# Kernel tuning notes

Hardware: AMD Instinct MI355X
Metric: run time of the kernel (lower is better)

Reference implementation:

```python
import jax, jax.numpy as jnp
import numpy as np

D_MODEL = 1024
NUM_HEADS = 16
DEPTH = D_MODEL // NUM_HEADS
B, S = 4, 1024


def setup_inputs() -> dict:
    key = jax.random.key(0)
    ks = jax.random.split(key, 12)
    sc = 1.0 / np.sqrt(D_MODEL)
    return {
        "v": jax.random.normal(ks[0], (B, S, D_MODEL), jnp.float32),
        "k": jax.random.normal(ks[1], (B, S, D_MODEL), jnp.float32),
        "q": jax.random.normal(ks[2], (B, S, D_MODEL), jnp.float32),
        "mask": jnp.zeros((B, 1, 1, S), jnp.float32),
        "adjoin_matrix": jax.random.normal(ks[3], (B, 1, S, S), jnp.float32),
        "wq_w": jax.random.normal(ks[4], (D_MODEL, D_MODEL), jnp.float32) * sc,
        "wq_b": jnp.zeros((D_MODEL,), jnp.float32),
        "wk_w": jax.random.normal(ks[5], (D_MODEL, D_MODEL), jnp.float32) * sc,
        "wk_b": jnp.zeros((D_MODEL,), jnp.float32),
        "wv_w": jax.random.normal(ks[6], (D_MODEL, D_MODEL), jnp.float32) * sc,
        "wv_b": jnp.zeros((D_MODEL,), jnp.float32),
        "dense_w": jax.random.normal(ks[7], (D_MODEL, D_MODEL), jnp.float32) * sc,
        "dense_b": jnp.zeros((D_MODEL,), jnp.float32),
    }


def _split_heads(x, batch):
    # [B, S, D] -> [B, H, S, depth]
    return x.reshape(batch, -1, NUM_HEADS, DEPTH).transpose(0, 2, 1, 3)


def reference(v, k, q, mask, adjoin_matrix,
              wq_w, wq_b, wk_w, wk_b, wv_w, wv_b, dense_w, dense_b):
    batch = q.shape[0]
    # torch nn.Linear: y = x @ W^T + b
    qh = _split_heads(q @ wq_w.T + wq_b, batch)
    kh = _split_heads(k @ wk_w.T + wk_b, batch)
    vh = _split_heads(v @ wv_w.T + wv_b, batch)

    logits = jnp.einsum('bhqd,bhkd->bhqk', qh, kh) / jnp.sqrt(
        jnp.asarray(DEPTH, qh.dtype))
    logits = logits + mask * (-1e9) + adjoin_matrix
    attn = jax.nn.softmax(logits, axis=-1).astype(qh.dtype)
    # dropout p=0 -> identity at inference
    ctx = jnp.einsum('bhqk,bhkd->bhqd', attn, vh)  # [B,H,S,depth]
    concat = ctx.transpose(0, 2, 1, 3).reshape(batch, -1, D_MODEL)
    out = concat @ dense_w.T + dense_b
    return out, attn
```

## Files before the change

### kernel.cpp

```cpp
#include <hip/hip_runtime.h>
#include <hip/hip_bf16.h>
#include <cstdint>
#include <cstddef>

#define B_ 4
#define S_ 1024
#define D_ 1024
#define H_ 16
#define DEPTH_ 64
#define M_ (B_*S_)

typedef __attribute__((ext_vector_type(4))) float f32x4;
typedef __attribute__((ext_vector_type(8))) __bf16 bf16x8;
typedef __attribute__((ext_vector_type(8))) unsigned short u16x8;
typedef __attribute__((ext_vector_type(4))) unsigned short u16x4;

typedef const __attribute__((address_space(1))) unsigned int GU32;
typedef __attribute__((address_space(3))) unsigned int LU32;

__device__ __forceinline__ unsigned short f2bf(float f) {
  unsigned int u = __builtin_bit_cast(unsigned int, f);
  u += 0x7FFFu + ((u >> 16) & 1u);
  return (unsigned short)(u >> 16);
}

__device__ __forceinline__ float bf2f(unsigned short v) {
  unsigned int u = (unsigned int)v << 16;
  return __builtin_bit_cast(float, u);
}

struct CvtAll { const float* s[7]; unsigned short* d[7]; };

__device__ __forceinline__ void cvt_body(const float* __restrict__ s,
                                         unsigned short* __restrict__ d, int i) {
  const f32x4* sp = (const f32x4*)s + (size_t)i * 2;
  f32x4 a = sp[0], b = sp[1];
  u16x8 o;
  o[0]=f2bf(a[0]); o[1]=f2bf(a[1]); o[2]=f2bf(a[2]); o[3]=f2bf(a[3]);
  o[4]=f2bf(b[0]); o[5]=f2bf(b[1]); o[6]=f2bf(b[2]); o[7]=f2bf(b[3]);
  *((u16x8*)d + i) = o;
}

__global__ void cvt_all_kernel(CvtAll a) {
  int bi = blockIdx.x, seg, i;
  if (bi < 6144) { seg = bi >> 11;              i = ((bi & 2047) << 8) + threadIdx.x; }
  else           { int t = bi - 6144; seg = 3 + (t >> 9); i = ((t & 511) << 8) + threadIdx.x; }
  cvt_body(a.s[seg], a.d[seg], i);
}

__device__ __forceinline__ void gemm_body(
    const unsigned short* __restrict__ A,
    const unsigned short* __restrict__ Bm,
    unsigned short* __restrict__ Obf,
    float* __restrict__ Of32,
    const float* __restrict__ bias,
    int N, int K, float scale, int biasRow, int m0, int n0)
{
  __shared__ unsigned short As[128*32];
  __shared__ unsigned short Bs[128*32];
  const int tid  = threadIdx.x;
  const int lane = tid & 63;
  const int w    = tid >> 6;
  const int wm   = w >> 1, wn = w & 1;
  const int fr   = lane & 15, kg = lane >> 4;

  f32x4 acc[4][4];
  #pragma unroll
  for (int i = 0; i < 4; ++i)
    #pragma unroll
    for (int j = 0; j < 4; ++j)
      acc[i][j] = (f32x4)0.0f;

  const int o0 = tid * 16,        o1 = (256 + tid) * 16;
  const int r0 = o0 >> 6,         c0 = (o0 & 63) >> 1;
  const int r1 = o1 >> 6,         c1 = (o1 & 63) >> 1;
  const int lds0 = (w * 64) * 16;
  const int lds1 = (256 + w * 64) * 16;

  const int nkt = K >> 5;
  for (int kt = 0; kt < nkt; ++kt) {
    const int kk = kt * 32;
    __builtin_amdgcn_global_load_lds((GU32*)(A  + (size_t)(m0 + r0) * K + kk + c0),
                                     (LU32*)((char*)As + lds0), 16, 0, 0);
    __builtin_amdgcn_global_load_lds((GU32*)(A  + (size_t)(m0 + r1) * K + kk + c1),
                                     (LU32*)((char*)As + lds1), 16, 0, 0);
    __builtin_amdgcn_global_load_lds((GU32*)(Bm + (size_t)(n0 + r0) * K + kk + c0),
                                     (LU32*)((char*)Bs + lds0), 16, 0, 0);
    __builtin_amdgcn_global_load_lds((GU32*)(Bm + (size_t)(n0 + r1) * K + kk + c1),
                                     (LU32*)((char*)Bs + lds1), 16, 0, 0);
    __syncthreads();

    bf16x8 af[4], bf[4];
    #pragma unroll
    for (int i = 0; i < 4; ++i)
      af[i] = *(const bf16x8*)&As[(wm * 64 + i * 16 + fr) * 32 + kg * 8];
    #pragma unroll
    for (int j = 0; j < 4; ++j)
      bf[j] = *(const bf16x8*)&Bs[(wn * 64 + j * 16 + fr) * 32 + kg * 8];
    #pragma unroll
    for (int i = 0; i < 4; ++i)
      #pragma unroll
      for (int j = 0; j < 4; ++j)
        acc[i][j] = __builtin_amdgcn_mfma_f32_16x16x32_bf16(af[i], bf[j], acc[i][j], 0, 0, 0);
    __syncthreads();
  }

  #pragma unroll
  for (int i = 0; i < 4; ++i) {
    const int rowb = m0 + wm * 64 + i * 16 + kg * 4;
    #pragma unroll
    for (int j = 0; j < 4; ++j) {
      const int col = n0 + wn * 64 + j * 16 + fr;
      const float bcol = biasRow ? 0.0f : bias[col];
      #pragma unroll
      for (int r = 0; r < 4; ++r) {
        const int row = rowb + r;
        const float bv = biasRow ? bias[row] : bcol;
        const float val = (acc[i][j][r] + bv) * scale;
        if (Obf) Obf[(size_t)row * N + col] = f2bf(val);
        else     Of32[(size_t)row * N + col] = val;
      }
    }
  }
}

struct GemmSet { const unsigned short* A; const unsigned short* Bm;
                 unsigned short* O; const float* bias; };

__launch_bounds__(256)
__global__ void qkv_gemm(GemmSet s0, GemmSet s1, GemmSet s2) {
  const int z = blockIdx.y;
  GemmSet s = (z == 0) ? s0 : (z == 1) ? s1 : s2;
  int m0, n0, N; float scale; int biasRow;
  if (z < 2) { m0 = (blockIdx.x & 31) * 128; n0 = (blockIdx.x >> 5) * 128;
               N = D_; scale = (z == 0) ? 0.125f : 1.0f; biasRow = 0; }
  else       { m0 = (blockIdx.x & 7) * 128;  n0 = (blockIdx.x >> 3) * 128;
               N = M_; scale = 1.0f; biasRow = 1; }
  gemm_body(s.A, s.Bm, s.O, nullptr, s.bias, N, D_, scale, biasRow, m0, n0);
}

__launch_bounds__(256)
__global__ void dense_gemm(const unsigned short* __restrict__ A,
                           const unsigned short* __restrict__ Bm,
                           float* __restrict__ O, const float* __restrict__ bias) {
  gemm_body(A, Bm, nullptr, O, bias, D_, D_, 1.0f, 0,
            blockIdx.x * 128, blockIdx.y * 128);
}

__launch_bounds__(512, 4)
__global__ void attn_kernel(const unsigned short* __restrict__ qp,
                            const unsigned short* __restrict__ kp,
                            const unsigned short* __restrict__ vt,
                            const float* __restrict__ mask,
                            const float* __restrict__ adjoin,
                            float* __restrict__ attn_out,
                            unsigned short* __restrict__ ctx)
{
  __shared__ __align__(16) char L[81920];
  char* const Pb = L;
  char* const Rg = L + 32768;

  const int tid = threadIdx.x, lane = tid & 63, w = tid >> 6;
  const int fr = lane & 15, kg = lane >> 4;
  const int fd = w & 3, kh = w >> 2;
  const int frsw = (fr & 7) << 4;
  const int r8 = lane >> 3;
  const int c7p = (((lane & 7) ^ r8) << 4);

  char* const Wb  = Rg + w * 6144;
  char* const Ks0 = Wb,        * const Ks1 = Wb + 2048;
  char* const Ab0 = Wb + 4096, * const Ab1 = Wb + 5120;

  const int i_ = blockIdx.x;
  const int bh = (i_ & 7) * 8 + ((i_ >> 3) & 7);
  const int qt = i_ >> 6;
  const int b = bh >> 4, h = bh & 15;
  const int q0 = qt * 16;
  const int kw = w * 128;

  const char* kG = (const char*)(kp + (size_t)b * S_ * D_ + h * DEPTH_);
  const char* aG = (const char*)(adjoin + (size_t)b * S_ * S_ + (size_t)q0 * S_);
  const char* vG = (const char*)(vt + (size_t)h * DEPTH_ * M_ + (size_t)b * S_);
  const char* mG = (const char*)(mask + (size_t)b * S_);

  auto stageK = [&](int t, char* dst) {
    #pragma unroll
    for (int j = 0; j < 2; ++j)
      __builtin_amdgcn_global_load_lds(
          (GU32*)(kG + (size_t)(kw + t * 16 + j * 8 + r8) * 2048 + c7p),
          (LU32*)(dst + j * 1024 + lane * 16), 16, 0, 0);
  };
  auto stageA = [&](int t, char* dst) {
    __builtin_amdgcn_global_load_lds(
        (GU32*)(aG + (size_t)(lane >> 2) * 4096 + kw * 4 + t * 64 + (lane & 3) * 16),
        (LU32*)(dst + lane * 16), 16, 0, 0);
  };
  auto stageV = [&](int t, char* dst) {
    #pragma unroll
    for (int j = 0; j < 2; ++j)
      __builtin_amdgcn_global_load_lds(
          (GU32*)(vG + (size_t)(fd * 16 + j * 8 + r8) * 8192 + kh * 1024 + t * 128 + c7p),
          (LU32*)(dst + j * 1024 + lane * 16), 16, 0, 0);
  };

  const unsigned short* qrow = qp + ((size_t)b * S_ + q0 + fr) * D_ + h * DEPTH_;
  bf16x8 qf0 = *(const bf16x8*)&qrow[kg * 8];
  bf16x8 qf1 = *(const bf16x8*)&qrow[32 + kg * 8];
  f32x4 mreg[8];
  #pragma unroll
  for (int t = 0; t < 8; ++t)
    mreg[t] = *(const f32x4*)(mG + kw * 4 + t * 64 + kg * 16);
  asm volatile("" ::: "memory");

  stageK(0, Ks0); stageA(0, Ab0);
  stageK(1, Ks1); stageA(1, Ab1);
  asm volatile("s_waitcnt vmcnt(3)" ::: "memory");
  __builtin_amdgcn_sched_barrier(0);

  float ls = 0.0f;

  #pragma unroll
  for (int t = 0; t < 8; ++t) {
    if (t == 7)     asm volatile("s_waitcnt vmcnt(2)" ::: "memory");
    else if (t > 0) asm volatile("s_waitcnt vmcnt(3)" ::: "memory");
    __builtin_amdgcn_sched_barrier(0);

    const char* kb = (t & 1) ? Ks1 : Ks0;
    const char* ab = (t & 1) ? Ab1 : Ab0;
    bf16x8 kf0 = *(const bf16x8*)(kb + fr * 128 + ((kg * 16) ^ frsw));
    bf16x8 kf1 = *(const bf16x8*)(kb + fr * 128 + ((64 + kg * 16) ^ frsw));
    f32x4 a4  = *(const f32x4*)(ab + fr * 64 + kg * 16);

    asm volatile("s_waitcnt lgkmcnt(0)" ::: "memory");
    __builtin_amdgcn_sched_barrier(0);

    if (t < 6)      { stageK(t + 2, (t & 1) ? Ks1 : Ks0);
                      stageA(t + 2, (t & 1) ? Ab1 : Ab0); }
    else if (t == 6)  stageV(0, Ks0);
    else              stageV(1, Ks1);

    f32x4 s = (f32x4)0.0f;
    s = __builtin_amdgcn_mfma_f32_16x16x32_bf16(kf0, qf0, s, 0, 0, 0);
    s = __builtin_amdgcn_mfma_f32_16x16x32_bf16(kf1, qf1, s, 0, 0, 0);

    f32x4 p;
    #pragma unroll
    for (int r = 0; r < 4; ++r)
      p[r] = __expf(s[r] + a4[r] + mreg[t][r] * (-1e9f));
    ls += (p[0] + p[1]) + (p[2] + p[3]);
    u16x4 pk;
    #pragma unroll
    for (int r = 0; r < 4; ++r) pk[r] = f2bf(p[r]);
    *(u16x4*)(Pb + fr * 2048 + ((kw * 2 + t * 32 + kg * 8) ^ frsw)) = pk;
  }

  ls += __shfl_xor(ls, 16);
  ls += __shfl_xor(ls, 32);
  if (lane < 16) *(float*)(Ab0 + lane * 4) = ls;

  asm volatile("s_waitcnt lgkmcnt(0)" ::: "memory");
  __builtin_amdgcn_s_barrier();
  __builtin_amdgcn_sched_barrier(0);

  f32x4 cacc = (f32x4)0.0f;
  #pragma unroll
  for (int t = 0; t < 8; ++t) {
    if (t == 7) asm volatile("s_waitcnt vmcnt(0)" ::: "memory");
    else        asm volatile("s_waitcnt vmcnt(2)" ::: "memory");
    __builtin_amdgcn_sched_barrier(0);

    const char* vb = (t & 1) ? Ks1 : Ks0;
    bf16x8 vf0 = *(const bf16x8*)(vb + fr * 128 + ((kg * 16) ^ frsw));
    bf16x8 vf1 = *(const bf16x8*)(vb + fr * 128 + ((64 + kg * 16) ^ frsw));
    bf16x8 pf0 = *(const bf16x8*)(Pb + fr * 2048 + ((kh * 1024 + t * 128 + kg * 16) ^ frsw));
    bf16x8 pf1 = *(const bf16x8*)(Pb + fr * 2048 + ((kh * 1024 + t * 128 + 64 + kg * 16) ^ frsw));

    asm volatile("s_waitcnt lgkmcnt(0)" ::: "memory");
    __builtin_amdgcn_sched_barrier(0);

    if (t < 6) stageV(t + 2, (t & 1) ? Ks1 : Ks0);

    cacc = __builtin_amdgcn_mfma_f32_16x16x32_bf16(vf0, pf0, cacc, 0, 0, 0);
    cacc = __builtin_amdgcn_mfma_f32_16x16x32_bf16(vf1, pf1, cacc, 0, 0, 0);
  }

  if (w >= 4) *(f32x4*)(Ab1 + lane * 16) = cacc;
  asm volatile("s_waitcnt lgkmcnt(0)" ::: "memory");
  __builtin_amdgcn_s_barrier();
  __builtin_amdgcn_sched_barrier(0);

  if (w < 4) {
    f32x4 red = *(const f32x4*)(Rg + (w + 4) * 6144 + 5120 + lane * 16);
    #pragma unroll
    for (int r = 0; r < 4; ++r) cacc[r] += red[r];
    float gs = 0.0f;
    #pragma unroll
    for (int w2 = 0; w2 < 8; ++w2)
      gs += *(const float*)(Rg + w2 * 6144 + 4096 + fr * 4);
    const float giC = 1.0f / gs;
    u16x4 cv;
    #pragma unroll
    for (int r = 0; r < 4; ++r) cv[r] = f2bf(cacc[r] * giC);
    *(u16x4*)&ctx[((size_t)b * S_ + q0 + fr) * D_ + h * DEPTH_ + fd * 16 + kg * 4] = cv;
  }

  #pragma unroll
  for (int j = 0; j < 2; ++j) {
    const int row = w * 2 + j;
    float gs = 0.0f;
    #pragma unroll
    for (int w2 = 0; w2 < 8; ++w2)
      gs += *(const float*)(Rg + w2 * 6144 + 4096 + row * 4);
    const float g = 1.0f / gs;
    const char* pr = Pb + row * 2048;
    const int rs = (row & 7) << 4;
    float* ao = attn_out + ((size_t)bh * S_ + q0 + row) * S_;
    #pragma unroll
    for (int half = 0; half < 2; ++half) {
      u16x8 pv = *(const u16x8*)(pr + ((half * 1024 + lane * 16) ^ rs));
      f32x4 o0, o1;
      #pragma unroll
      for (int e = 0; e < 4; ++e) { o0[e] = bf2f(pv[e]) * g; o1[e] = bf2f(pv[4 + e]) * g; }
      __builtin_nontemporal_store(o0, (f32x4*)(ao + half * 512 + lane * 8));
      __builtin_nontemporal_store(o1, (f32x4*)(ao + half * 512 + lane * 8 + 4));
    }
  }
}

extern "C" void kernel_launch(void* const* d_in, const int* in_sizes, int n_in,
                              void* d_out, int out_size, void* d_ws, size_t ws_size,
                              hipStream_t stream)
{
  const float* v_in   = (const float*)d_in[0];
  const float* k_in   = (const float*)d_in[1];
  const float* q_in   = (const float*)d_in[2];
  const float* mask   = (const float*)d_in[3];
  const float* adjoin = (const float*)d_in[4];
  const float* wq_w   = (const float*)d_in[5];
  const float* wq_b   = (const float*)d_in[6];
  const float* wk_w   = (const float*)d_in[7];
  const float* wk_b   = (const float*)d_in[8];
  const float* wv_w   = (const float*)d_in[9];
  const float* wv_b   = (const float*)d_in[10];
  const float* wd_w   = (const float*)d_in[11];
  const float* wd_b   = (const float*)d_in[12];

  unsigned short* xq  = (unsigned short*)d_ws;
  unsigned short* xk  = xq  + (size_t)M_ * D_;
  unsigned short* xv  = xk  + (size_t)M_ * D_;
  unsigned short* wqb = xv  + (size_t)M_ * D_;
  unsigned short* wkb = wqb + (size_t)D_ * D_;
  unsigned short* wvb = wkb + (size_t)D_ * D_;
  unsigned short* wdb = wvb + (size_t)D_ * D_;
  unsigned short* qp  = wdb + (size_t)D_ * D_;
  unsigned short* kp  = qp  + (size_t)M_ * D_;
  unsigned short* vt  = kp  + (size_t)M_ * D_;
  unsigned short* ctx = vt  + (size_t)M_ * D_;

  float* out  = (float*)d_out;
  float* attn = out + (size_t)B_ * S_ * D_;

  CvtAll ca;
  ca.s[0] = q_in; ca.s[1] = k_in; ca.s[2] = v_in;
  ca.s[3] = wq_w; ca.s[4] = wk_w; ca.s[5] = wv_w; ca.s[6] = wd_w;
  ca.d[0] = xq;   ca.d[1] = xk;   ca.d[2] = xv;
  ca.d[3] = wqb;  ca.d[4] = wkb;  ca.d[5] = wvb;  ca.d[6] = wdb;
  cvt_all_kernel<<<8192, 256, 0, stream>>>(ca);

  GemmSet sq{xq,  wqb, qp, wq_b};
  GemmSet sk{xk,  wkb, kp, wk_b};
  GemmSet sv{wvb, xv,  vt, wv_b};
  qkv_gemm<<<dim3(256, 3), 256, 0, stream>>>(sq, sk, sv);

  attn_kernel<<<B_ * H_ * (S_ / 16), 512, 0, stream>>>(qp, kp, vt, mask, adjoin, attn, ctx);

  dense_gemm<<<dim3(32, 8), 256, 0, stream>>>(ctx, wdb, out, wd_b);
}
```

Measured before the change: 186.8 us.

## Load K, adjoin, mask and V straight into registers instead of LDS staging

```diff
diff --git a/kernel.cpp b/kernel.cpp
--- a/kernel.cpp
+++ b/kernel.cpp
@@ -156,20 +156,15 @@
                             float* __restrict__ attn_out,
                             unsigned short* __restrict__ ctx)
 {
-  __shared__ __align__(16) char L[81920];
+  __shared__ __align__(16) char L[37376];
   char* const Pb = L;
-  char* const Rg = L + 32768;
+  float* const ssum = (float*)(L + 32768);
+  char* const Red = L + 33280;
 
   const int tid = threadIdx.x, lane = tid & 63, w = tid >> 6;
   const int fr = lane & 15, kg = lane >> 4;
   const int fd = w & 3, kh = w >> 2;
   const int frsw = (fr & 7) << 4;
-  const int r8 = lane >> 3;
-  const int c7p = (((lane & 7) ^ r8) << 4);
-
-  char* const Wb  = Rg + w * 6144;
-  char* const Ks0 = Wb,        * const Ks1 = Wb + 2048;
-  char* const Ab0 = Wb + 4096, * const Ab1 = Wb + 5120;
 
   const int i_ = blockIdx.x;
   const int bh = (i_ & 7) * 8 + ((i_ >> 3) & 7);
@@ -183,121 +178,77 @@
   const char* vG = (const char*)(vt + (size_t)h * DEPTH_ * M_ + (size_t)b * S_);
   const char* mG = (const char*)(mask + (size_t)b * S_);
 
-  auto stageK = [&](int t, char* dst) {
-    #pragma unroll
-    for (int j = 0; j < 2; ++j)
-      __builtin_amdgcn_global_load_lds(
-          (GU32*)(kG + (size_t)(kw + t * 16 + j * 8 + r8) * 2048 + c7p),
-          (LU32*)(dst + j * 1024 + lane * 16), 16, 0, 0);
-  };
-  auto stageA = [&](int t, char* dst) {
-    __builtin_amdgcn_global_load_lds(
-        (GU32*)(aG + (size_t)(lane >> 2) * 4096 + kw * 4 + t * 64 + (lane & 3) * 16),
-        (LU32*)(dst + lane * 16), 16, 0, 0);
-  };
-  auto stageV = [&](int t, char* dst) {
-    #pragma unroll
-    for (int j = 0; j < 2; ++j)
-      __builtin_amdgcn_global_load_lds(
-          (GU32*)(vG + (size_t)(fd * 16 + j * 8 + r8) * 8192 + kh * 1024 + t * 128 + c7p),
-          (LU32*)(dst + j * 1024 + lane * 16), 16, 0, 0);
-  };
+  const char* kA = kG + (size_t)(kw + fr) * 2048 + kg * 16;
+  const char* aA = aG + (size_t)fr * 4096 + kw * 4 + kg * 16;
+  const char* mA = mG + kw * 4 + kg * 16;
+  const char* vA = vG + (size_t)(fd * 16 + fr) * 8192 + kh * 1024 + kg * 16;
 
   const unsigned short* qrow = qp + ((size_t)b * S_ + q0 + fr) * D_ + h * DEPTH_;
   bf16x8 qf0 = *(const bf16x8*)&qrow[kg * 8];
   bf16x8 qf1 = *(const bf16x8*)&qrow[32 + kg * 8];
-  f32x4 mreg[8];
-  #pragma unroll
-  for (int t = 0; t < 8; ++t)
-    mreg[t] = *(const f32x4*)(mG + kw * 4 + t * 64 + kg * 16);
-  asm volatile("" ::: "memory");
-
-  stageK(0, Ks0); stageA(0, Ab0);
-  stageK(1, Ks1); stageA(1, Ab1);
-  asm volatile("s_waitcnt vmcnt(3)" ::: "memory");
-  __builtin_amdgcn_sched_barrier(0);
-
+
+  bf16x8 kf0c = *(const bf16x8*)(kA);
+  bf16x8 kf1c = *(const bf16x8*)(kA + 64);
+  f32x4  a4c  = *(const f32x4*)(aA);
+  f32x4  m4c  = *(const f32x4*)(mA);
   float ls = 0.0f;
-
   #pragma unroll
   for (int t = 0; t < 8; ++t) {
-    if (t == 7)     asm volatile("s_waitcnt vmcnt(2)" ::: "memory");
-    else if (t > 0) asm volatile("s_waitcnt vmcnt(3)" ::: "memory");
-    __builtin_amdgcn_sched_barrier(0);
-
-    const char* kb = (t & 1) ? Ks1 : Ks0;
-    const char* ab = (t & 1) ? Ab1 : Ab0;
-    bf16x8 kf0 = *(const bf16x8*)(kb + fr * 128 + ((kg * 16) ^ frsw));
-    bf16x8 kf1 = *(const bf16x8*)(kb + fr * 128 + ((64 + kg * 16) ^ frsw));
-    f32x4 a4  = *(const f32x4*)(ab + fr * 64 + kg * 16);
-
-    asm volatile("s_waitcnt lgkmcnt(0)" ::: "memory");
-    __builtin_amdgcn_sched_barrier(0);
-
-    if (t < 6)      { stageK(t + 2, (t & 1) ? Ks1 : Ks0);
-                      stageA(t + 2, (t & 1) ? Ab1 : Ab0); }
-    else if (t == 6)  stageV(0, Ks0);
-    else              stageV(1, Ks1);
+    const int tn = (t < 7) ? t + 1 : 7;
+    bf16x8 kf0n = *(const bf16x8*)(kA + (size_t)tn * 32768);
+    bf16x8 kf1n = *(const bf16x8*)(kA + (size_t)tn * 32768 + 64);
+    f32x4  a4n  = *(const f32x4*)(aA + tn * 64);
+    f32x4  m4n  = *(const f32x4*)(mA + tn * 64);
 
     f32x4 s = (f32x4)0.0f;
-    s = __builtin_amdgcn_mfma_f32_16x16x32_bf16(kf0, qf0, s, 0, 0, 0);
-    s = __builtin_amdgcn_mfma_f32_16x16x32_bf16(kf1, qf1, s, 0, 0, 0);
+    s = __builtin_amdgcn_mfma_f32_16x16x32_bf16(kf0c, qf0, s, 0, 0, 0);
+    s = __builtin_amdgcn_mfma_f32_16x16x32_bf16(kf1c, qf1, s, 0, 0, 0);
 
     f32x4 p;
     #pragma unroll
     for (int r = 0; r < 4; ++r)
-      p[r] = __expf(s[r] + a4[r] + mreg[t][r] * (-1e9f));
+      p[r] = __expf(s[r] + a4c[r] + m4c[r] * (-1e9f));
     ls += (p[0] + p[1]) + (p[2] + p[3]);
     u16x4 pk;
     #pragma unroll
     for (int r = 0; r < 4; ++r) pk[r] = f2bf(p[r]);
     *(u16x4*)(Pb + fr * 2048 + ((kw * 2 + t * 32 + kg * 8) ^ frsw)) = pk;
+
+    kf0c = kf0n; kf1c = kf1n; a4c = a4n; m4c = m4n;
   }
 
   ls += __shfl_xor(ls, 16);
   ls += __shfl_xor(ls, 32);
-  if (lane < 16) *(float*)(Ab0 + lane * 4) = ls;
-
-  asm volatile("s_waitcnt lgkmcnt(0)" ::: "memory");
-  __builtin_amdgcn_s_barrier();
-  __builtin_amdgcn_sched_barrier(0);
+  if (lane < 16) ssum[lane * 8 + w] = ls;
+
+  __syncthreads();
 
   f32x4 cacc = (f32x4)0.0f;
+  bf16x8 vf0c = *(const bf16x8*)(vA);
+  bf16x8 vf1c = *(const bf16x8*)(vA + 64);
   #pragma unroll
   for (int t = 0; t < 8; ++t) {
-    if (t == 7) asm volatile("s_waitcnt vmcnt(0)" ::: "memory");
-    else        asm volatile("s_waitcnt vmcnt(2)" ::: "memory");
-    __builtin_amdgcn_sched_barrier(0);
-
-    const char* vb = (t & 1) ? Ks1 : Ks0;
-    bf16x8 vf0 = *(const bf16x8*)(vb + fr * 128 + ((kg * 16) ^ frsw));
-    bf16x8 vf1 = *(const bf16x8*)(vb + fr * 128 + ((64 + kg * 16) ^ frsw));
+    const int tn = (t < 7) ? t + 1 : 7;
+    bf16x8 vf0n = *(const bf16x8*)(vA + tn * 128);
+    bf16x8 vf1n = *(const bf16x8*)(vA + tn * 128 + 64);
     bf16x8 pf0 = *(const bf16x8*)(Pb + fr * 2048 + ((kh * 1024 + t * 128 + kg * 16) ^ frsw));
     bf16x8 pf1 = *(const bf16x8*)(Pb + fr * 2048 + ((kh * 1024 + t * 128 + 64 + kg * 16) ^ frsw));
-
-    asm volatile("s_waitcnt lgkmcnt(0)" ::: "memory");
-    __builtin_amdgcn_sched_barrier(0);
-
-    if (t < 6) stageV(t + 2, (t & 1) ? Ks1 : Ks0);
-
-    cacc = __builtin_amdgcn_mfma_f32_16x16x32_bf16(vf0, pf0, cacc, 0, 0, 0);
-    cacc = __builtin_amdgcn_mfma_f32_16x16x32_bf16(vf1, pf1, cacc, 0, 0, 0);
-  }
-
-  if (w >= 4) *(f32x4*)(Ab1 + lane * 16) = cacc;
-  asm volatile("s_waitcnt lgkmcnt(0)" ::: "memory");
-  __builtin_amdgcn_s_barrier();
-  __builtin_amdgcn_sched_barrier(0);
+    cacc = __builtin_amdgcn_mfma_f32_16x16x32_bf16(vf0c, pf0, cacc, 0, 0, 0);
+    cacc = __builtin_amdgcn_mfma_f32_16x16x32_bf16(vf1c, pf1, cacc, 0, 0, 0);
+    vf0c = vf0n; vf1c = vf1n;
+  }
+
+  if (w >= 4) *(f32x4*)(Red + fd * 1024 + lane * 16) = cacc;
+  __syncthreads();
 
   if (w < 4) {
-    f32x4 red = *(const f32x4*)(Rg + (w + 4) * 6144 + 5120 + lane * 16);
+    f32x4 red = *(const f32x4*)(Red + fd * 1024 + lane * 16);
     #pragma unroll
     for (int r = 0; r < 4; ++r) cacc[r] += red[r];
-    float gs = 0.0f;
-    #pragma unroll
-    for (int w2 = 0; w2 < 8; ++w2)
-      gs += *(const float*)(Rg + w2 * 6144 + 4096 + fr * 4);
-    const float giC = 1.0f / gs;
+    f32x4 sa = *(const f32x4*)&ssum[fr * 8];
+    f32x4 sb = *(const f32x4*)&ssum[fr * 8 + 4];
+    const float giC = 1.0f / ((sa[0] + sa[1]) + (sa[2] + sa[3]) +
+                              ((sb[0] + sb[1]) + (sb[2] + sb[3])));
     u16x4 cv;
     #pragma unroll
     for (int r = 0; r < 4; ++r) cv[r] = f2bf(cacc[r] * giC);
@@ -307,11 +258,10 @@
   #pragma unroll
   for (int j = 0; j < 2; ++j) {
     const int row = w * 2 + j;
-    float gs = 0.0f;
-    #pragma unroll
-    for (int w2 = 0; w2 < 8; ++w2)
-      gs += *(const float*)(Rg + w2 * 6144 + 4096 + row * 4);
-    const float g = 1.0f / gs;
+    f32x4 ta = *(const f32x4*)&ssum[row * 8];
+    f32x4 tb = *(const f32x4*)&ssum[row * 8 + 4];
+    const float g = 1.0f / ((ta[0] + ta[1]) + (ta[2] + ta[3]) +
+                            ((tb[0] + tb[1]) + (tb[2] + tb[3])));
     const char* pr = Pb + row * 2048;
     const int rs = (row & 7) << 4;
     float* ao = attn_out + ((size_t)bh * S_ + q0 + row) * S_;
```

After: 269.2 us. 44.1% more time.

## Deepen attention K/adjoin/V staging to four buffers with register prefetch

Applied to the files above, without the earlier changes.

```diff
diff --git a/kernel.cpp b/kernel.cpp
--- a/kernel.cpp
+++ b/kernel.cpp
@@ -147,7 +147,7 @@
             blockIdx.x * 128, blockIdx.y * 128);
 }
 
-__launch_bounds__(512, 4)
+__launch_bounds__(512, 2)
 __global__ void attn_kernel(const unsigned short* __restrict__ qp,
                             const unsigned short* __restrict__ kp,
                             const unsigned short* __restrict__ vt,
@@ -156,9 +156,11 @@
                             float* __restrict__ attn_out,
                             unsigned short* __restrict__ ctx)
 {
-  __shared__ __align__(16) char L[81920];
+  __shared__ __align__(16) char L[135680];
   char* const Pb = L;
   char* const Rg = L + 32768;
+  float* const Ssum = (float*)(L + 131072);
+  char* const Red = L + 131584;
 
   const int tid = threadIdx.x, lane = tid & 63, w = tid >> 6;
   const int fr = lane & 15, kg = lane >> 4;
@@ -167,9 +169,13 @@
   const int r8 = lane >> 3;
   const int c7p = (((lane & 7) ^ r8) << 4);
 
-  char* const Wb  = Rg + w * 6144;
-  char* const Ks0 = Wb,        * const Ks1 = Wb + 2048;
-  char* const Ab0 = Wb + 4096, * const Ab1 = Wb + 5120;
+  char* const Wb = Rg + w * 12288;
+  char* const Kb0 = Wb,         * const Kb1 = Wb + 2048;
+  char* const Kb2 = Wb + 4096,  * const Kb3 = Wb + 6144;
+  char* const Ab0 = Wb + 8192,  * const Ab1 = Wb + 9216;
+  char* const Ab2 = Wb + 10240, * const Ab3 = Wb + 11264;
+  char* const KB[4] = {Kb0, Kb1, Kb2, Kb3};
+  char* const AB[4] = {Ab0, Ab1, Ab2, Ab3};
 
   const int i_ = blockIdx.x;
   const int bh = (i_ & 7) * 8 + ((i_ >> 3) & 7);
@@ -212,92 +218,116 @@
     mreg[t] = *(const f32x4*)(mG + kw * 4 + t * 64 + kg * 16);
   asm volatile("" ::: "memory");
 
-  stageK(0, Ks0); stageA(0, Ab0);
-  stageK(1, Ks1); stageA(1, Ab1);
-  asm volatile("s_waitcnt vmcnt(3)" ::: "memory");
+  stageK(0, Kb0); stageA(0, Ab0);
+  stageK(1, Kb1); stageA(1, Ab1);
+  stageK(2, Kb2); stageA(2, Ab2);
+  stageK(3, Kb3); stageA(3, Ab3);
+  asm volatile("s_waitcnt vmcnt(9)" ::: "memory");
   __builtin_amdgcn_sched_barrier(0);
 
+  bf16x8 kf0c = *(const bf16x8*)(Kb0 + fr * 128 + ((kg * 16) ^ frsw));
+  bf16x8 kf1c = *(const bf16x8*)(Kb0 + fr * 128 + ((64 + kg * 16) ^ frsw));
+  f32x4  a4c  = *(const f32x4*)(Ab0 + fr * 64 + kg * 16);
+
   float ls = 0.0f;
 
   #pragma unroll
   for (int t = 0; t < 8; ++t) {
-    if (t == 7)     asm volatile("s_waitcnt vmcnt(2)" ::: "memory");
-    else if (t > 0) asm volatile("s_waitcnt vmcnt(3)" ::: "memory");
-    __builtin_amdgcn_sched_barrier(0);
-
-    const char* kb = (t & 1) ? Ks1 : Ks0;
-    const char* ab = (t & 1) ? Ab1 : Ab0;
-    bf16x8 kf0 = *(const bf16x8*)(kb + fr * 128 + ((kg * 16) ^ frsw));
-    bf16x8 kf1 = *(const bf16x8*)(kb + fr * 128 + ((64 + kg * 16) ^ frsw));
-    f32x4 a4  = *(const f32x4*)(ab + fr * 64 + kg * 16);
-
     asm volatile("s_waitcnt lgkmcnt(0)" ::: "memory");
     __builtin_amdgcn_sched_barrier(0);
 
-    if (t < 6)      { stageK(t + 2, (t & 1) ? Ks1 : Ks0);
-                      stageA(t + 2, (t & 1) ? Ab1 : Ab0); }
-    else if (t == 6)  stageV(0, Ks0);
-    else              stageV(1, Ks1);
+    if (t + 4 <= 7) { stageK(t + 4, KB[t & 3]); stageA(t + 4, AB[t & 3]); }
+
+    bf16x8 kf0n, kf1n; f32x4 a4n;
+    if (t < 7) {
+      if (t <= 3)      asm volatile("s_waitcnt vmcnt(9)" ::: "memory");
+      else if (t == 4) asm volatile("s_waitcnt vmcnt(6)" ::: "memory");
+      else if (t == 5) asm volatile("s_waitcnt vmcnt(3)" ::: "memory");
+      else             asm volatile("s_waitcnt vmcnt(0)" ::: "memory");
+      __builtin_amdgcn_sched_barrier(0);
+      const char* kb = KB[(t + 1) & 3];
+      const char* ab = AB[(t + 1) & 3];
+      kf0n = *(const bf16x8*)(kb + fr * 128 + ((kg * 16) ^ frsw));
+      kf1n = *(const bf16x8*)(kb + fr * 128 + ((64 + kg * 16) ^ frsw));
+      a4n  = *(const f32x4*)(ab + fr * 64 + kg * 16);
+    }
 
     f32x4 s = (f32x4)0.0f;
-    s = __builtin_amdgcn_mfma_f32_16x16x32_bf16(kf0, qf0, s, 0, 0, 0);
-    s = __builtin_amdgcn_mfma_f32_16x16x32_bf16(kf1, qf1, s, 0, 0, 0);
-
+    s = __builtin_amdgcn_mfma_f32_16x16x32_bf16(kf0c, qf0, s, 0, 0, 0);
+    s = __builtin_amdgcn_mfma_f32_16x16x32_bf16(kf1c, qf1, s, 0, 0, 0);
     f32x4 p;
     #pragma unroll
     for (int r = 0; r < 4; ++r)
-      p[r] = __expf(s[r] + a4[r] + mreg[t][r] * (-1e9f));
+      p[r] = __expf(s[r] + a4c[r] + mreg[t][r] * (-1e9f));
     ls += (p[0] + p[1]) + (p[2] + p[3]);
     u16x4 pk;
     #pragma unroll
     for (int r = 0; r < 4; ++r) pk[r] = f2bf(p[r]);
     *(u16x4*)(Pb + fr * 2048 + ((kw * 2 + t * 32 + kg * 8) ^ frsw)) = pk;
-  }
+
+    if (t < 7) { kf0c = kf0n; kf1c = kf1n; a4c = a4n; }
+  }
+
+  asm volatile("s_waitcnt lgkmcnt(0)" ::: "memory");
+  __builtin_amdgcn_sched_barrier(0);
+  stageV(0, Kb0); stageV(1, Kb1); stageV(2, Kb2); stageV(3, Kb3);
 
   ls += __shfl_xor(ls, 16);
   ls += __shfl_xor(ls, 32);
-  if (lane < 16) *(float*)(Ab0 + lane * 4) = ls;
+  if (lane < 16) Ssum[lane * 8 + w] = ls;
 
   asm volatile("s_waitcnt lgkmcnt(0)" ::: "memory");
   __builtin_amdgcn_s_barrier();
   __builtin_amdgcn_sched_barrier(0);
 
+  asm volatile("s_waitcnt vmcnt(6)" ::: "memory");
+  __builtin_amdgcn_sched_barrier(0);
+  bf16x8 vf0c = *(const bf16x8*)(Kb0 + fr * 128 + ((kg * 16) ^ frsw));
+  bf16x8 vf1c = *(const bf16x8*)(Kb0 + fr * 128 + ((64 + kg * 16) ^ frsw));
+  bf16x8 pf0c = *(const bf16x8*)(Pb + fr * 2048 + ((kh * 1024 + kg * 16) ^ frsw));
+  bf16x8 pf1c = *(const bf16x8*)(Pb + fr * 2048 + ((kh * 1024 + 64 + kg * 16) ^ frsw));
+
   f32x4 cacc = (f32x4)0.0f;
   #pragma unroll
   for (int t = 0; t < 8; ++t) {
-    if (t == 7) asm volatile("s_waitcnt vmcnt(0)" ::: "memory");
-    else        asm volatile("s_waitcnt vmcnt(2)" ::: "memory");
-    __builtin_amdgcn_sched_barrier(0);
-
-    const char* vb = (t & 1) ? Ks1 : Ks0;
-    bf16x8 vf0 = *(const bf16x8*)(vb + fr * 128 + ((kg * 16) ^ frsw));
-    bf16x8 vf1 = *(const bf16x8*)(vb + fr * 128 + ((64 + kg * 16) ^ frsw));
-    bf16x8 pf0 = *(const bf16x8*)(Pb + fr * 2048 + ((kh * 1024 + t * 128 + kg * 16) ^ frsw));
-    bf16x8 pf1 = *(const bf16x8*)(Pb + fr * 2048 + ((kh * 1024 + t * 128 + 64 + kg * 16) ^ frsw));
-
     asm volatile("s_waitcnt lgkmcnt(0)" ::: "memory");
     __builtin_amdgcn_sched_barrier(0);
 
-    if (t < 6) stageV(t + 2, (t & 1) ? Ks1 : Ks0);
-
-    cacc = __builtin_amdgcn_mfma_f32_16x16x32_bf16(vf0, pf0, cacc, 0, 0, 0);
-    cacc = __builtin_amdgcn_mfma_f32_16x16x32_bf16(vf1, pf1, cacc, 0, 0, 0);
-  }
-
-  if (w >= 4) *(f32x4*)(Ab1 + lane * 16) = cacc;
+    if (t + 4 <= 7) stageV(t + 4, KB[t & 3]);
+
+    bf16x8 vf0n, vf1n, pf0n, pf1n;
+    if (t < 7) {
+      if (t <= 3)      asm volatile("s_waitcnt vmcnt(6)" ::: "memory");
+      else if (t == 4) asm volatile("s_waitcnt vmcnt(4)" ::: "memory");
+      else if (t == 5) asm volatile("s_waitcnt vmcnt(2)" ::: "memory");
+      else             asm volatile("s_waitcnt vmcnt(0)" ::: "memory");
+      __builtin_amdgcn_sched_barrier(0);
+      const char* vb = KB[(t + 1) & 3];
+      vf0n = *(const bf16x8*)(vb + fr * 128 + ((kg * 16) ^ frsw));
+      vf1n = *(const bf16x8*)(vb + fr * 128 + ((64 + kg * 16) ^ frsw));
+      pf0n = *(const bf16x8*)(Pb + fr * 2048 + ((kh * 1024 + (t + 1) * 128 + kg * 16) ^ frsw));
+      pf1n = *(const bf16x8*)(Pb + fr * 2048 + ((kh * 1024 + (t + 1) * 128 + 64 + kg * 16) ^ frsw));
+    }
+
+    cacc = __builtin_amdgcn_mfma_f32_16x16x32_bf16(vf0c, pf0c, cacc, 0, 0, 0);
+    cacc = __builtin_amdgcn_mfma_f32_16x16x32_bf16(vf1c, pf1c, cacc, 0, 0, 0);
+
+    if (t < 7) { vf0c = vf0n; vf1c = vf1n; pf0c = pf0n; pf1c = pf1n; }
+  }
+
+  if (w >= 4) *(f32x4*)(Red + fd * 1024 + lane * 16) = cacc;
   asm volatile("s_waitcnt lgkmcnt(0)" ::: "memory");
   __builtin_amdgcn_s_barrier();
   __builtin_amdgcn_sched_barrier(0);
 
   if (w < 4) {
-    f32x4 red = *(const f32x4*)(Rg + (w + 4) * 6144 + 5120 + lane * 16);
+    f32x4 red = *(const f32x4*)(Red + fd * 1024 + lane * 16);
     #pragma unroll
     for (int r = 0; r < 4; ++r) cacc[r] += red[r];
-    float gs = 0.0f;
-    #pragma unroll
-    for (int w2 = 0; w2 < 8; ++w2)
-      gs += *(const float*)(Rg + w2 * 6144 + 4096 + fr * 4);
-    const float giC = 1.0f / gs;
+    f32x4 sa = *(const f32x4*)&Ssum[fr * 8];
+    f32x4 sb = *(const f32x4*)&Ssum[fr * 8 + 4];
+    const float giC = 1.0f / ((sa[0] + sa[1]) + (sa[2] + sa[3]) +
+                              ((sb[0] + sb[1]) + (sb[2] + sb[3])));
     u16x4 cv;
     #pragma unroll
     for (int r = 0; r < 4; ++r) cv[r] = f2bf(cacc[r] * giC);
@@ -307,11 +337,10 @@
   #pragma unroll
   for (int j = 0; j < 2; ++j) {
     const int row = w * 2 + j;
-    float gs = 0.0f;
-    #pragma unroll
-    for (int w2 = 0; w2 < 8; ++w2)
-      gs += *(const float*)(Rg + w2 * 6144 + 4096 + row * 4);
-    const float g = 1.0f / gs;
+    f32x4 ta = *(const f32x4*)&Ssum[row * 8];
+    f32x4 tb = *(const f32x4*)&Ssum[row * 8 + 4];
+    const float g = 1.0f / ((ta[0] + ta[1]) + (ta[2] + ta[3]) +
+                            ((tb[0] + tb[1]) + (tb[2] + tb[3])));
     const char* pr = Pb + row * 2048;
     const int rs = (row & 7) << 4;
     float* ao = attn_out + ((size_t)bh * S_ + q0 + row) * S_;
```

Result: slower. 209.9 us (+12.4%).

## Fuse fp32-to-bf16 conversion of q and k into the QKV GEMM loads

Applied to the files above, without the earlier changes.

```diff
diff --git a/kernel.cpp b/kernel.cpp
--- a/kernel.cpp
+++ b/kernel.cpp
@@ -29,7 +29,7 @@
   return __builtin_bit_cast(float, u);
 }
 
-struct CvtAll { const float* s[7]; unsigned short* d[7]; };
+struct CvtAll { const float* s[5]; unsigned short* d[5]; };
 
 __device__ __forceinline__ void cvt_body(const float* __restrict__ s,
                                          unsigned short* __restrict__ d, int i) {
@@ -43,13 +43,15 @@
 
 __global__ void cvt_all_kernel(CvtAll a) {
   int bi = blockIdx.x, seg, i;
-  if (bi < 6144) { seg = bi >> 11;              i = ((bi & 2047) << 8) + threadIdx.x; }
-  else           { int t = bi - 6144; seg = 3 + (t >> 9); i = ((t & 511) << 8) + threadIdx.x; }
+  if (bi < 2048) { seg = 0;                i = (bi << 8) + threadIdx.x; }
+  else { int t = bi - 2048; seg = 1 + (t >> 9); i = ((t & 511) << 8) + threadIdx.x; }
   cvt_body(a.s[seg], a.d[seg], i);
 }
 
+template<bool AF32>
 __device__ __forceinline__ void gemm_body(
-    const unsigned short* __restrict__ A,
+    const unsigned short* __restrict__ Abf,
+    const float* __restrict__ Af32,
     const unsigned short* __restrict__ Bm,
     unsigned short* __restrict__ Obf,
     float* __restrict__ Of32,
@@ -80,14 +82,31 @@
   const int nkt = K >> 5;
   for (int kt = 0; kt < nkt; ++kt) {
     const int kk = kt * 32;
-    __builtin_amdgcn_global_load_lds((GU32*)(A  + (size_t)(m0 + r0) * K + kk + c0),
-                                     (LU32*)((char*)As + lds0), 16, 0, 0);
-    __builtin_amdgcn_global_load_lds((GU32*)(A  + (size_t)(m0 + r1) * K + kk + c1),
-                                     (LU32*)((char*)As + lds1), 16, 0, 0);
     __builtin_amdgcn_global_load_lds((GU32*)(Bm + (size_t)(n0 + r0) * K + kk + c0),
                                      (LU32*)((char*)Bs + lds0), 16, 0, 0);
     __builtin_amdgcn_global_load_lds((GU32*)(Bm + (size_t)(n0 + r1) * K + kk + c1),
                                      (LU32*)((char*)Bs + lds1), 16, 0, 0);
+    if constexpr (AF32) {
+      const int ar = m0 + (tid >> 1);
+      const int ac = (tid & 1) * 16;
+      const float* as_ = Af32 + (size_t)ar * K + kk + ac;
+      f32x4 a0 = *(const f32x4*)(as_);
+      f32x4 a1 = *(const f32x4*)(as_ + 4);
+      f32x4 a2 = *(const f32x4*)(as_ + 8);
+      f32x4 a3 = *(const f32x4*)(as_ + 12);
+      u16x8 q0, q1;
+      q0[0]=f2bf(a0[0]); q0[1]=f2bf(a0[1]); q0[2]=f2bf(a0[2]); q0[3]=f2bf(a0[3]);
+      q0[4]=f2bf(a1[0]); q0[5]=f2bf(a1[1]); q0[6]=f2bf(a1[2]); q0[7]=f2bf(a1[3]);
+      q1[0]=f2bf(a2[0]); q1[1]=f2bf(a2[1]); q1[2]=f2bf(a2[2]); q1[3]=f2bf(a2[3]);
+      q1[4]=f2bf(a3[0]); q1[5]=f2bf(a3[1]); q1[6]=f2bf(a3[2]); q1[7]=f2bf(a3[3]);
+      *(u16x8*)((char*)As + tid * 32)      = q0;
+      *(u16x8*)((char*)As + tid * 32 + 16) = q1;
+    } else {
+      __builtin_amdgcn_global_load_lds((GU32*)(Abf + (size_t)(m0 + r0) * K + kk + c0),
+                                       (LU32*)((char*)As + lds0), 16, 0, 0);
+      __builtin_amdgcn_global_load_lds((GU32*)(Abf + (size_t)(m0 + r1) * K + kk + c1),
+                                       (LU32*)((char*)As + lds1), 16, 0, 0);
+    }
     __syncthreads();
 
     bf16x8 af[4], bf[4];
@@ -124,27 +143,30 @@
   }
 }
 
-struct GemmSet { const unsigned short* A; const unsigned short* Bm;
-                 unsigned short* O; const float* bias; };
+struct GemmSet { const unsigned short* A; const float* Af;
+                 const unsigned short* Bm; unsigned short* O; const float* bias; };
 
 __launch_bounds__(256)
 __global__ void qkv_gemm(GemmSet s0, GemmSet s1, GemmSet s2) {
   const int z = blockIdx.y;
   GemmSet s = (z == 0) ? s0 : (z == 1) ? s1 : s2;
-  int m0, n0, N; float scale; int biasRow;
-  if (z < 2) { m0 = (blockIdx.x & 31) * 128; n0 = (blockIdx.x >> 5) * 128;
-               N = D_; scale = (z == 0) ? 0.125f : 1.0f; biasRow = 0; }
-  else       { m0 = (blockIdx.x & 7) * 128;  n0 = (blockIdx.x >> 3) * 128;
-               N = M_; scale = 1.0f; biasRow = 1; }
-  gemm_body(s.A, s.Bm, s.O, nullptr, s.bias, N, D_, scale, biasRow, m0, n0);
+  if (z < 2) {
+    const int m0 = (blockIdx.x & 31) * 128, n0 = (blockIdx.x >> 5) * 128;
+    gemm_body<true>(nullptr, s.Af, s.Bm, s.O, nullptr, s.bias, D_, D_,
+                    (z == 0) ? 0.125f : 1.0f, 0, m0, n0);
+  } else {
+    const int m0 = (blockIdx.x & 7) * 128,  n0 = (blockIdx.x >> 3) * 128;
+    gemm_body<false>(s.A, nullptr, s.Bm, s.O, nullptr, s.bias, M_, D_,
+                     1.0f, 1, m0, n0);
+  }
 }
 
 __launch_bounds__(256)
 __global__ void dense_gemm(const unsigned short* __restrict__ A,
                            const unsigned short* __restrict__ Bm,
                            float* __restrict__ O, const float* __restrict__ bias) {
-  gemm_body(A, Bm, nullptr, O, bias, D_, D_, 1.0f, 0,
-            blockIdx.x * 128, blockIdx.y * 128);
+  gemm_body<false>(A, nullptr, Bm, nullptr, O, bias, D_, D_, 1.0f, 0,
+                   blockIdx.x * 128, blockIdx.y * 128);
 }
 
 __launch_bounds__(512, 4)
@@ -239,9 +261,11 @@
     else if (t == 6)  stageV(0, Ks0);
     else              stageV(1, Ks1);
 
+    __builtin_amdgcn_s_setprio(1);
     f32x4 s = (f32x4)0.0f;
     s = __builtin_amdgcn_mfma_f32_16x16x32_bf16(kf0, qf0, s, 0, 0, 0);
     s = __builtin_amdgcn_mfma_f32_16x16x32_bf16(kf1, qf1, s, 0, 0, 0);
+    __builtin_amdgcn_s_setprio(0);
 
     f32x4 p;
     #pragma unroll
@@ -280,8 +304,10 @@
 
     if (t < 6) stageV(t + 2, (t & 1) ? Ks1 : Ks0);
 
+    __builtin_amdgcn_s_setprio(1);
     cacc = __builtin_amdgcn_mfma_f32_16x16x32_bf16(vf0, pf0, cacc, 0, 0, 0);
     cacc = __builtin_amdgcn_mfma_f32_16x16x32_bf16(vf1, pf1, cacc, 0, 0, 0);
+    __builtin_amdgcn_s_setprio(0);
   }
 
   if (w >= 4) *(f32x4*)(Ab1 + lane * 16) = cacc;
@@ -361,15 +387,13 @@
   float* attn = out + (size_t)B_ * S_ * D_;
 
   CvtAll ca;
-  ca.s[0] = q_in; ca.s[1] = k_in; ca.s[2] = v_in;
-  ca.s[3] = wq_w; ca.s[4] = wk_w; ca.s[5] = wv_w; ca.s[6] = wd_w;
-  ca.d[0] = xq;   ca.d[1] = xk;   ca.d[2] = xv;
-  ca.d[3] = wqb;  ca.d[4] = wkb;  ca.d[5] = wvb;  ca.d[6] = wdb;
-  cvt_all_kernel<<<8192, 256, 0, stream>>>(ca);
-
-  GemmSet sq{xq,  wqb, qp, wq_b};
-  GemmSet sk{xk,  wkb, kp, wk_b};
-  GemmSet sv{wvb, xv,  vt, wv_b};
+  ca.s[0] = v_in; ca.s[1] = wq_w; ca.s[2] = wk_w; ca.s[3] = wv_w; ca.s[4] = wd_w;
+  ca.d[0] = xv;   ca.d[1] = wqb;  ca.d[2] = wkb;  ca.d[3] = wvb;  ca.d[4] = wdb;
+  cvt_all_kernel<<<4096, 256, 0, stream>>>(ca);
+
+  GemmSet sq{nullptr, q_in, wqb, qp, wq_b};
+  GemmSet sk{nullptr, k_in, wkb, kp, wk_b};
+  GemmSet sv{wvb, nullptr, xv,  vt, wv_b};
   qkv_gemm<<<dim3(256, 3), 256, 0, stream>>>(sq, sk, sv);
 
   attn_kernel<<<B_ * H_ * (S_ / 16), 512, 0, stream>>>(qp, kp, vt, mask, adjoin, attn, ctx);
```

Result: no change. 184.1 us (-1.5%).
